# Kernel optimization log

Hardware: AMD Instinct MI355X
Metric: run time of the kernel (lower is better)

The kernel has to match this reference:

```python
import jax, jax.numpy as jnp
import numpy as np

NUM_HEADS = 12
EPS = 1e-12  # torch F.normalize clamp_min eps


def _l2norm(t):
    return t / jnp.clip(jnp.linalg.norm(t, axis=-1, keepdims=True), EPS)


def setup_inputs() -> dict:
    key = jax.random.key(0)
    ks = jax.random.split(key, 6)
    B, N, C = 8, 4096, 768
    Nc, Nb, F = 1, 512, 16
    s = 0.02
    return {
        "x": jax.random.normal(ks[0], (B, N, C), jnp.float32),
        "bank": jax.random.normal(ks[1], (Nc, Nb, F), jnp.float32),
        "Wq": jax.random.normal(ks[2], (C, C), jnp.float32) * s,
        "Wkv": jax.random.normal(ks[3], (F, 2 * C), jnp.float32) * s,
        "Wlin": jax.random.normal(ks[4], (C, C), jnp.float32) * s,
        "b_lin": jnp.zeros((C,), jnp.float32),
        "prelu_a": jnp.asarray(0.25, jnp.float32),
        "temperature": jnp.ones((NUM_HEADS, 1, 1), jnp.float32),
    }


def reference(x, bank, Wq, Wkv, Wlin, b_lin, prelu_a, temperature):
    B, N, C = x.shape
    Nc, Nb, _ = bank.shape
    H = NUM_HEADS
    d = C // H
    # q: (B, H, N, d), L2-normalized along d
    q = _l2norm((x @ Wq).reshape(B, N, H, d).transpose(0, 2, 1, 3))
    # kv from (detached) bank: (2, Nc, H, Nb, d)
    kv = (bank @ Wkv).reshape(Nc, Nb, 2, H, d).transpose(2, 0, 3, 1, 4)
    k = _l2norm(kv[0])
    v = kv[1]
    # cosine attention with per-head learned temperature: (B, Nc, H, N, Nb)
    attn = jnp.einsum('bhnd,chmd->bchnm', q, k) * temperature
    attn = jax.nn.softmax(attn, axis=-1)
    # (dropout is identity in eval mode)
    out = jnp.einsum('bchnm,chmd->bchnd', attn, v)  # (B, Nc, H, N, d)
    out = out.reshape(B * Nc, H, N, d).transpose(0, 2, 1, 3).reshape(B, N, C)
    out = out @ Wlin + b_lin
    # PReLU with a single shared parameter
    return jnp.where(out >= 0, out, prelu_a * out)
```

## Files before the change

kernel.cpp:

```cpp
#include <hip/hip_runtime.h>
#include <cstdint>
#include <cstddef>

typedef unsigned short u16;
typedef __attribute__((ext_vector_type(8))) __bf16 bf16x8;
typedef __attribute__((ext_vector_type(4))) float f32x4;

#define MFMA(a, b, c) __builtin_amdgcn_mfma_f32_16x16x32_bf16(a, b, c, 0, 0, 0)

__device__ __forceinline__ u16 f2bf(float f) {
  union { float f; uint32_t u; } x; x.f = f;
  uint32_t r = x.u + 0x7fffu + ((x.u >> 16) & 1u);
  return (u16)(r >> 16);
}

__device__ __forceinline__ void gld16(const u16* g, u16* l) {
  __builtin_amdgcn_global_load_lds(
      (const __attribute__((address_space(1))) void*)g,
      (__attribute__((address_space(3))) void*)l, 16, 0, 0);
}

__global__ void cvt_f32_bf16(const float* __restrict__ src, u16* __restrict__ dst, int n4) {
  int i = blockIdx.x * blockDim.x + threadIdx.x;
  int stride = gridDim.x * blockDim.x;
  for (; i < n4; i += stride) {
    float4 v = ((const float4*)src)[i];
    ushort4 o;
    o.x = f2bf(v.x); o.y = f2bf(v.y); o.z = f2bf(v.z); o.w = f2bf(v.w);
    ((ushort4*)dst)[i] = o;
  }
}

__global__ void transpose_cvt(const float* __restrict__ src, u16* __restrict__ dst, int R, int C) {
  __shared__ float tile[32][33];
  int bx = blockIdx.x * 32, by = blockIdx.y * 32;
  int tx = threadIdx.x, ty = threadIdx.y;
  #pragma unroll
  for (int i = ty; i < 32; i += 8)
    tile[i][tx] = src[(size_t)(by + i) * C + bx + tx];
  __syncthreads();
  #pragma unroll
  for (int i = ty; i < 32; i += 8)
    dst[(size_t)(bx + i) * R + by + tx] = f2bf(tile[tx][i]);
}

__global__ void kv_prep(const float* __restrict__ bank, const float* __restrict__ Wkv,
                        const float* __restrict__ temp, u16* __restrict__ K, u16* __restrict__ VT) {
  int m = blockIdx.x & 511, h = blockIdx.x >> 9;
  int j = threadIdx.x;
  const float* br = bank + m * 16;
  float kj = 0.f, vj = 0.f;
  #pragma unroll
  for (int f = 0; f < 16; ++f) {
    float bv = br[f];
    kj = fmaf(bv, Wkv[f * 1536 + h * 64 + j], kj);
    vj = fmaf(bv, Wkv[f * 1536 + 768 + h * 64 + j], vj);
  }
  float ss = kj * kj;
  #pragma unroll
  for (int o = 32; o; o >>= 1) ss += __shfl_xor(ss, o);
  float rn = rsqrtf(fmaxf(ss, 1e-24f));
  K[((size_t)h * 512 + m) * 64 + j] = f2bf(kj * rn * temp[h] * 1.4426950408889634f);
  VT[((size_t)h * 64 + j) * 512 + m] = f2bf(vj);
}

template <int MODE>
__global__ __launch_bounds__(256, 3) void gemm_bt(
    const u16* __restrict__ A, const u16* __restrict__ BT, void* __restrict__ Cout,
    int M, int N, int K, const float* __restrict__ bias, const float* __restrict__ prelu) {
  __shared__ u16 sA[2][128 * 32];
  __shared__ u16 sB[2][128 * 32];
  const int ntiles = N >> 7;
  const int swz = (blockIdx.x & 7) * (gridDim.x >> 3) + (blockIdx.x >> 3);
  const int m0 = (swz / ntiles) << 7;
  const int n0 = (swz % ntiles) << 7;
  const int tid = threadIdx.x;
  const int w = tid >> 6, lane = tid & 63;
  const int wm = (w >> 1) << 6, wn = (w & 1) << 6;
  const int srow = lane >> 2, scol = (lane & 3) << 3;
  const u16* ga = A + (size_t)(m0 + (w << 5) + srow) * K + scol;
  const u16* gb = BT + (size_t)(n0 + (w << 5) + srow) * K + scol;
  const int lofs = (w << 5) * 32;
  const int fr = lane & 15, fq = (lane >> 4) << 3;
  f32x4 acc[4][4] = {};

  auto stage = [&](int buf, int k0) {
    gld16(ga + k0, sA[buf] + lofs);
    gld16(ga + k0 + (size_t)16 * K, sA[buf] + lofs + 16 * 32);
    gld16(gb + k0, sB[buf] + lofs);
    gld16(gb + k0 + (size_t)16 * K, sB[buf] + lofs + 16 * 32);
  };

  stage(0, 0);
  __syncthreads();
  int cur = 0;
  for (int k0 = 0; k0 < K; k0 += 32) {
    if (k0 + 32 < K) stage(cur ^ 1, k0 + 32);
    bf16x8 af[4], bfr[4];
    #pragma unroll
    for (int t = 0; t < 4; ++t) {
      af[t] = *(const bf16x8*)(sA[cur] + (wm + t * 16 + fr) * 32 + fq);
      bfr[t] = *(const bf16x8*)(sB[cur] + (wn + t * 16 + fr) * 32 + fq);
    }
    #pragma unroll
    for (int i = 0; i < 4; ++i)
      #pragma unroll
      for (int j = 0; j < 4; ++j)
        acc[i][j] = MFMA(af[i], bfr[j], acc[i][j]);
    __syncthreads();
    cur ^= 1;
  }

  const int q = lane >> 4;
  float a = (MODE == 1) ? prelu[0] : 0.f;
  #pragma unroll
  for (int tm = 0; tm < 4; ++tm)
    #pragma unroll
    for (int tn = 0; tn < 4; ++tn) {
      int col = n0 + wn + tn * 16 + fr;
      float bv = (MODE == 1) ? bias[col] : 0.f;
      #pragma unroll
      for (int r = 0; r < 4; ++r) {
        int row = m0 + wm + tm * 16 + q * 4 + r;
        float v = acc[tm][tn][r];
        if (MODE == 1) {
          v += bv;
          v = v >= 0.f ? v : v * a;
          ((float*)Cout)[(size_t)row * N + col] = v;
        } else {
          ((u16*)Cout)[(size_t)row * N + col] = f2bf(v);
        }
      }
    }
}

__global__ __launch_bounds__(512, 4) void attn_kern(
    const u16* __restrict__ Q, const u16* __restrict__ Kb,
    const u16* __restrict__ Vt, u16* __restrict__ O) {
  __shared__ __align__(16) u16 sK[2][64 * 72];
  __shared__ __align__(16) u16 sV[2][64 * 72];

  const int qb = blockIdx.x & 127;
  const int h = blockIdx.x >> 7;
  const int tid = threadIdx.x, w = tid >> 6, lane = tid & 63;
  const int fr = lane & 15, quad = lane >> 4;
  const int rowbase = qb * 256 + (w << 5);

  bf16x8 qa[2][2];
  #pragma unroll
  for (int g = 0; g < 2; ++g) {
    const u16* qp = Q + (size_t)(rowbase + g * 16 + fr) * 768 + h * 64 + (quad << 3);
    qa[g][0] = *(const bf16x8*)qp;
    qa[g][1] = *(const bf16x8*)(qp + 32);
    float ss = 0.f;
    #pragma unroll
    for (int j = 0; j < 8; ++j) {
      float f0 = (float)qa[g][0][j], f1 = (float)qa[g][1][j];
      ss += f0 * f0 + f1 * f1;
    }
    ss += __shfl_xor(ss, 16);
    ss += __shfl_xor(ss, 32);
    float rn = rsqrtf(fmaxf(ss, 1e-24f));
    #pragma unroll
    for (int j = 0; j < 8; ++j) {
      qa[g][0][j] = (__bf16)((float)qa[g][0][j] * rn);
      qa[g][1][j] = (__bf16)((float)qa[g][1][j] * rn);
    }
  }

  const u16* kg = Kb + (size_t)h * 512 * 64;
  const u16* vg = Vt + (size_t)h * 64 * 512;
  int4 kreg, vreg;
  auto load_chunk = [&](int c) {
    kreg = *(const int4*)(kg + (size_t)(c * 64 + (tid >> 3)) * 64 + (tid & 7) * 8);
    vreg = *(const int4*)(vg + (size_t)(tid >> 3) * 512 + c * 64 + (tid & 7) * 8);
  };
  auto store_chunk = [&](int buf) {
    *(int4*)(sK[buf] + (tid >> 3) * 72 + (tid & 7) * 8) = kreg;
    *(int4*)(sV[buf] + (tid >> 3) * 72 + (tid & 7) * 8) = vreg;
  };

  load_chunk(0);
  store_chunk(0);
  load_chunk(1);
  __syncthreads();

  f32x4 oa[2][4] = {};
  float ls[2] = {0.f, 0.f};

  for (int c = 0; c < 8; ++c) {
    const int cb = c & 1;
    if (c < 7) store_chunk((c + 1) & 1);
    if (c < 6) load_chunk(c + 2);

    #pragma unroll
    for (int ks = 0; ks < 2; ++ks) {
      f32x4 s[2][2];
      #pragma unroll
      for (int half = 0; half < 2; ++half) {
        const int mt = ks * 2 + half;
        const u16* kp = sK[cb] + (mt * 16 + fr) * 72 + (quad << 3);
        bf16x8 ak0 = *(const bf16x8*)kp;
        bf16x8 ak1 = *(const bf16x8*)(kp + 32);
        #pragma unroll
        for (int g = 0; g < 2; ++g) {
          f32x4 z = {0.f, 0.f, 0.f, 0.f};
          z = MFMA(ak0, qa[g][0], z);
          z = MFMA(ak1, qa[g][1], z);
          s[g][half] = z;
        }
      }
      bf16x8 pbf[2];
      #pragma unroll
      for (int g = 0; g < 2; ++g)
        #pragma unroll
        for (int half = 0; half < 2; ++half)
          #pragma unroll
          for (int r = 0; r < 4; ++r) {
            float p = __builtin_amdgcn_exp2f(s[g][half][r]);
            ls[g] += p;
            pbf[g][half * 4 + r] = (__bf16)p;
          }
      #pragma unroll
      for (int t = 0; t < 4; ++t) {
        const u16* vp = sV[cb] + (t * 16 + fr) * 72 + ks * 32 + (quad << 2);
        bf16x8 va;
        *(uint2*)&va = *(const uint2*)vp;
        *((uint2*)&va + 1) = *(const uint2*)(vp + 16);
        #pragma unroll
        for (int g = 0; g < 2; ++g)
          oa[g][t] = MFMA(va, pbf[g], oa[g][t]);
      }
    }
    __syncthreads();
  }

  #pragma unroll
  for (int g = 0; g < 2; ++g) {
    float l = ls[g];
    l += __shfl_xor(l, 16);
    l += __shfl_xor(l, 32);
    float rl = __builtin_amdgcn_rcpf(l);
    u16* op = O + (size_t)(rowbase + g * 16 + fr) * 768 + h * 64 + (quad << 2);
    #pragma unroll
    for (int t = 0; t < 4; ++t) {
      ushort4 pk;
      pk.x = f2bf(oa[g][t][0] * rl);
      pk.y = f2bf(oa[g][t][1] * rl);
      pk.z = f2bf(oa[g][t][2] * rl);
      pk.w = f2bf(oa[g][t][3] * rl);
      *(ushort4*)(op + t * 16) = pk;
    }
  }
}

extern "C" void kernel_launch(void* const* d_in, const int* in_sizes, int n_in,
                              void* d_out, int out_size, void* d_ws, size_t ws_size,
                              hipStream_t stream) {
  const float* x      = (const float*)d_in[0];
  const float* bank   = (const float*)d_in[1];
  const float* Wq     = (const float*)d_in[2];
  const float* Wkv    = (const float*)d_in[3];
  const float* Wlin   = (const float*)d_in[4];
  const float* b_lin  = (const float*)d_in[5];
  const float* prelu  = (const float*)d_in[6];
  const float* temp   = (const float*)d_in[7];
  float* out = (float*)d_out;

  char* ws = (char*)d_ws;
  const size_t NELEM = 25165824;
  u16* qbuf  = (u16*)ws;
  u16* xbuf  = (u16*)(ws + 50331648);
  u16* obuf  = xbuf;
  u16* wqt   = (u16*)(ws + 100663296);
  u16* wlt   = wqt + 589824;
  u16* kbuf  = wlt + 589824;
  u16* vtbuf = kbuf + 393216;

  cvt_f32_bf16<<<4096, 256, 0, stream>>>(x, xbuf, (int)(NELEM / 4));
  transpose_cvt<<<dim3(24, 24), dim3(32, 8), 0, stream>>>(Wq, wqt, 768, 768);
  transpose_cvt<<<dim3(24, 24), dim3(32, 8), 0, stream>>>(Wlin, wlt, 768, 768);
  kv_prep<<<6144, 64, 0, stream>>>(bank, Wkv, temp, kbuf, vtbuf);
  gemm_bt<0><<<1536, 256, 0, stream>>>(xbuf, wqt, qbuf, 32768, 768, 768, nullptr, nullptr);
  attn_kern<<<1536, 512, 0, stream>>>(qbuf, kbuf, vtbuf, obuf);
  gemm_bt<1><<<1536, 256, 0, stream>>>(obuf, wlt, out, 32768, 768, 768, b_lin, prelu);
}
```

Measured before the change: 370.3 us.

## Load full K head into LDS once, read V from global, merge transposes

Measured after the change: 490.4 us. +32.5%, slower.

```diff
diff --git a/kernel.cpp b/kernel.cpp
--- a/kernel.cpp
+++ b/kernel.cpp
@@ -31,7 +31,11 @@
   }
 }
 
-__global__ void transpose_cvt(const float* __restrict__ src, u16* __restrict__ dst, int R, int C) {
+__global__ void transpose_cvt2(const float* __restrict__ s0, u16* __restrict__ d0,
+                               const float* __restrict__ s1, u16* __restrict__ d1,
+                               int R, int C) {
+  const float* src = blockIdx.z ? s1 : s0;
+  u16* dst = blockIdx.z ? d1 : d0;
   __shared__ float tile[32][33];
   int bx = blockIdx.x * 32, by = blockIdx.y * 32;
   int tx = threadIdx.x, ty = threadIdx.y;
@@ -137,8 +141,7 @@
 __global__ __launch_bounds__(512, 4) void attn_kern(
     const u16* __restrict__ Q, const u16* __restrict__ Kb,
     const u16* __restrict__ Vt, u16* __restrict__ O) {
-  __shared__ __align__(16) u16 sK[2][64 * 72];
-  __shared__ __align__(16) u16 sV[2][64 * 72];
+  __shared__ __align__(16) u16 sK[512 * 72];
 
   const int qb = blockIdx.x & 127;
   const int h = blockIdx.x >> 7;
@@ -146,6 +149,12 @@
   const int fr = lane & 15, quad = lane >> 4;
   const int rowbase = qb * 256 + (w << 5);
 
+  const u16* kg = Kb + (size_t)h * 512 * 64;
+  int4 kreg[8];
+  #pragma unroll
+  for (int j = 0; j < 8; ++j)
+    kreg[j] = *(const int4*)(kg + (size_t)tid * 64 + j * 8);
+
   bf16x8 qa[2][2];
   #pragma unroll
   for (int g = 0; g < 2; ++g) {
@@ -168,38 +177,23 @@
     }
   }
 
-  const u16* kg = Kb + (size_t)h * 512 * 64;
+  #pragma unroll
+  for (int j = 0; j < 8; ++j)
+    *(int4*)(sK + tid * 72 + j * 8) = kreg[j];
+  __syncthreads();
+
   const u16* vg = Vt + (size_t)h * 64 * 512;
-  int4 kreg, vreg;
-  auto load_chunk = [&](int c) {
-    kreg = *(const int4*)(kg + (size_t)(c * 64 + (tid >> 3)) * 64 + (tid & 7) * 8);
-    vreg = *(const int4*)(vg + (size_t)(tid >> 3) * 512 + c * 64 + (tid & 7) * 8);
-  };
-  auto store_chunk = [&](int buf) {
-    *(int4*)(sK[buf] + (tid >> 3) * 72 + (tid & 7) * 8) = kreg;
-    *(int4*)(sV[buf] + (tid >> 3) * 72 + (tid & 7) * 8) = vreg;
-  };
-
-  load_chunk(0);
-  store_chunk(0);
-  load_chunk(1);
-  __syncthreads();
-
   f32x4 oa[2][4] = {};
-  float ls[2] = {0.f, 0.f};
+  f32x4 lsv[2] = {};
 
   for (int c = 0; c < 8; ++c) {
-    const int cb = c & 1;
-    if (c < 7) store_chunk((c + 1) & 1);
-    if (c < 6) load_chunk(c + 2);
-
     #pragma unroll
     for (int ks = 0; ks < 2; ++ks) {
       f32x4 s[2][2];
       #pragma unroll
       for (int half = 0; half < 2; ++half) {
         const int mt = ks * 2 + half;
-        const u16* kp = sK[cb] + (mt * 16 + fr) * 72 + (quad << 3);
+        const u16* kp = sK + (size_t)(c * 64 + mt * 16 + fr) * 72 + (quad << 3);
         bf16x8 ak0 = *(const bf16x8*)kp;
         bf16x8 ak1 = *(const bf16x8*)(kp + 32);
         #pragma unroll
@@ -210,34 +204,41 @@
           s[g][half] = z;
         }
       }
+      uint2 vlo[4], vhi[4];
+      #pragma unroll
+      for (int t = 0; t < 4; ++t) {
+        const u16* vpg = vg + (size_t)(t * 16 + fr) * 512 + c * 64 + ks * 32 + (quad << 2);
+        vlo[t] = *(const uint2*)vpg;
+        vhi[t] = *(const uint2*)(vpg + 16);
+      }
       bf16x8 pbf[2];
       #pragma unroll
       for (int g = 0; g < 2; ++g)
         #pragma unroll
-        for (int half = 0; half < 2; ++half)
+        for (int half = 0; half < 2; ++half) {
+          f32x4 pv;
           #pragma unroll
           for (int r = 0; r < 4; ++r) {
-            float p = __builtin_amdgcn_exp2f(s[g][half][r]);
-            ls[g] += p;
-            pbf[g][half * 4 + r] = (__bf16)p;
+            pv[r] = __builtin_amdgcn_exp2f(s[g][half][r]);
+            pbf[g][half * 4 + r] = (__bf16)pv[r];
           }
+          lsv[g] += pv;
+        }
       #pragma unroll
       for (int t = 0; t < 4; ++t) {
-        const u16* vp = sV[cb] + (t * 16 + fr) * 72 + ks * 32 + (quad << 2);
         bf16x8 va;
-        *(uint2*)&va = *(const uint2*)vp;
-        *((uint2*)&va + 1) = *(const uint2*)(vp + 16);
+        *(uint2*)&va = vlo[t];
+        *((uint2*)&va + 1) = vhi[t];
         #pragma unroll
         for (int g = 0; g < 2; ++g)
           oa[g][t] = MFMA(va, pbf[g], oa[g][t]);
       }
     }
-    __syncthreads();
   }
 
   #pragma unroll
   for (int g = 0; g < 2; ++g) {
-    float l = ls[g];
+    float l = lsv[g][0] + lsv[g][1] + lsv[g][2] + lsv[g][3];
     l += __shfl_xor(l, 16);
     l += __shfl_xor(l, 32);
     float rl = __builtin_amdgcn_rcpf(l);
@@ -278,8 +279,7 @@
   u16* vtbuf = kbuf + 393216;
 
   cvt_f32_bf16<<<4096, 256, 0, stream>>>(x, xbuf, (int)(NELEM / 4));
-  transpose_cvt<<<dim3(24, 24), dim3(32, 8), 0, stream>>>(Wq, wqt, 768, 768);
-  transpose_cvt<<<dim3(24, 24), dim3(32, 8), 0, stream>>>(Wlin, wlt, 768, 768);
+  transpose_cvt2<<<dim3(24, 24, 2), dim3(32, 8), 0, stream>>>(Wq, wqt, Wlin, wlt, 768, 768);
   kv_prep<<<6144, 64, 0, stream>>>(bank, Wkv, temp, kbuf, vtbuf);
   gemm_bt<0><<<1536, 256, 0, stream>>>(xbuf, wqt, qbuf, 32768, 768, 768, nullptr, nullptr);
   attn_kern<<<1536, 512, 0, stream>>>(qbuf, kbuf, vtbuf, obuf);
```
